# Kernel tuning notes

Hardware: AMD Instinct MI355X
Metric: run time of the kernel (lower is better)

## Reference

```python
import jax, jax.numpy as jnp
import numpy as np

DIM, HEADS, DHEAD, CTX_DIM, FF_MULT = 320, 8, 40, 768, 4
INNER_FF = FF_MULT * DIM  # 1280
EPS = 1e-5


def layer_norm(x, g, b):
    mu = jnp.mean(x, axis=-1, keepdims=True)
    var = jnp.mean((x - mu) ** 2, axis=-1, keepdims=True)
    return (x - mu) * jax.lax.rsqrt(var + EPS) * g + b


def attention(x, ctx, wq, wk, wv, wo, bo):
    # x: [b, i, DIM], ctx: [b, j, c]
    b, i, _ = x.shape
    j = ctx.shape[1]
    q = (x @ wq).reshape(b, i, HEADS, DHEAD)
    k = (ctx @ wk).reshape(b, j, HEADS, DHEAD)
    v = (ctx @ wv).reshape(b, j, HEADS, DHEAD)
    scale = DHEAD ** -0.5
    sim = jnp.einsum('bihd,bjhd->bhij', q, k) * scale  # full NxN, non-flash
    attn = jax.nn.softmax(sim, axis=-1)
    out = jnp.einsum('bhij,bjhd->bihd', attn, v).reshape(b, i, HEADS * DHEAD)
    return out @ wo + bo


def setup_inputs() -> dict:
    key = jax.random.key(0)
    ks = jax.random.split(key, 24)
    nrm = lambda k, shp, fan: jax.random.normal(k, shp, jnp.float32) * (fan ** -0.5)
    d = {
        'x': jax.random.normal(ks[0], (1, 4096, DIM), jnp.float32),
        'context': jax.random.normal(ks[1], (1, 77, CTX_DIM), jnp.float32),
        'n1_g': jnp.ones((DIM,), jnp.float32), 'n1_b': jnp.zeros((DIM,), jnp.float32),
        'a1_wq': nrm(ks[2], (DIM, DIM), DIM), 'a1_wk': nrm(ks[3], (DIM, DIM), DIM),
        'a1_wv': nrm(ks[4], (DIM, DIM), DIM), 'a1_wo': nrm(ks[5], (DIM, DIM), DIM),
        'a1_bo': jnp.zeros((DIM,), jnp.float32),
        'n2_g': jnp.ones((DIM,), jnp.float32), 'n2_b': jnp.zeros((DIM,), jnp.float32),
        'a2_wq': nrm(ks[6], (DIM, DIM), DIM), 'a2_wk': nrm(ks[7], (CTX_DIM, DIM), CTX_DIM),
        'a2_wv': nrm(ks[8], (CTX_DIM, DIM), CTX_DIM), 'a2_wo': nrm(ks[9], (DIM, DIM), DIM),
        'a2_bo': jnp.zeros((DIM,), jnp.float32),
        'n3_g': jnp.ones((DIM,), jnp.float32), 'n3_b': jnp.zeros((DIM,), jnp.float32),
        'ff_w1': nrm(ks[10], (DIM, 2 * INNER_FF), DIM),
        'ff_b1': jnp.zeros((2 * INNER_FF,), jnp.float32),
        'ff_w2': nrm(ks[11], (INNER_FF, DIM), INNER_FF),
        'ff_b2': jnp.zeros((DIM,), jnp.float32),
    }
    return d


def reference(x, context, n1_g, n1_b, a1_wq, a1_wk, a1_wv, a1_wo, a1_bo,
              n2_g, n2_b, a2_wq, a2_wk, a2_wv, a2_wo, a2_bo,
              n3_g, n3_b, ff_w1, ff_b1, ff_w2, ff_b2):
    # self-attention
    x = attention(layer_norm(x, n1_g, n1_b), layer_norm(x, n1_g, n1_b),
                  a1_wq, a1_wk, a1_wv, a1_wo, a1_bo) + x
    # cross-attention with text context
    x = attention(layer_norm(x, n2_g, n2_b), context,
                  a2_wq, a2_wk, a2_wv, a2_wo, a2_bo) + x
    # GEGLU feed-forward
    h = layer_norm(x, n3_g, n3_b) @ ff_w1 + ff_b1
    val, gate = jnp.split(h, 2, axis=-1)
    x = (val * jax.nn.gelu(gate, approximate=False)) @ ff_w2 + ff_b2 + x
    return x
```

## Files before the change

kernel.cpp:

```cpp
#include <hip/hip_runtime.h>
#include <hip/hip_bf16.h>
#include <math.h>

typedef __bf16 bf16;
typedef __attribute__((ext_vector_type(8))) __bf16 bf16x8;
typedef __attribute__((ext_vector_type(4))) __bf16 bf16x4;
typedef __attribute__((ext_vector_type(4))) float f32x4;
typedef __attribute__((ext_vector_type(2))) float f32x2;
typedef __attribute__((ext_vector_type(4))) short shortx4;

#define NTOK 4096
#define DIM  320
#define HEADS 8
#define DHEAD 40
#define NCTX 77
#define CTXD 768
#define IFF  1280

#define QSCALE (0.15811388300841897f * 1.4426950408889634f)

__device__ __forceinline__ bf16x8 bzero8() {
    bf16x8 v;
#pragma unroll
    for (int e = 0; e < 8; ++e) v[e] = (bf16)0.0f;
    return v;
}

__device__ __forceinline__ void gld_lds16(const void* g, void* l) {
    __builtin_amdgcn_global_load_lds(
        (const __attribute__((address_space(1))) void*)g,
        (__attribute__((address_space(3))) void*)l, 16, 0, 0);
}

#define PRE_TILES 2280
#define CONV_BLOCKS 231

struct PreJob { const float* src; bf16* dst; int K, N, ntx, tile0, perm; };
struct PreTab { PreJob j[10]; };

__global__ __launch_bounds__(256)
void preprocess_all(PreTab P, const float* __restrict__ ctx, bf16* __restrict__ ctxb) {
    const int b = blockIdx.x;
    const int tx = threadIdx.x, ty = threadIdx.y;
    if (b >= PRE_TILES) {
        int i = (b - PRE_TILES) * 256 + ty * 32 + tx;
        if (i < NCTX * CTXD) ctxb[i] = (bf16)ctx[i];
        return;
    }
    int ji = 0;
#pragma unroll
    for (int k = 1; k < 10; ++k)
        if (b >= P.j[k].tile0) ji = k;
    const PreJob jb = P.j[ji];
    const int local = b - jb.tile0;
    const int n0 = (local % jb.ntx) * 32;
    const int k0 = (local / jb.ntx) * 32;

    __shared__ float tile[32][33];
#pragma unroll
    for (int i = 0; i < 4; ++i)
        tile[ty + i * 8][tx] = jb.src[(size_t)(k0 + ty + i * 8) * jb.N + n0 + tx];
    __syncthreads();
#pragma unroll
    for (int i = 0; i < 4; ++i) {
        int n = n0 + ty + i * 8;
        int nd = jb.perm ? ((n < 1280) ? 2 * n : 2 * (n - 1280) + 1) : n;
        jb.dst[(size_t)nd * jb.K + k0 + tx] = (bf16)tile[tx][ty + i * 8];
    }
}

__device__ __forceinline__ void ln_body(const float* __restrict__ X, const float* __restrict__ g,
                                        const float* __restrict__ b, bf16* __restrict__ Y, int row) {
    int lane = threadIdx.x & 63;
    const float* xr = X + (size_t)row * DIM;
    float v[5];
    float sum = 0.f;
#pragma unroll
    for (int c = 0; c < 5; ++c) { v[c] = xr[c * 64 + lane]; sum += v[c]; }
#pragma unroll
    for (int off = 1; off < 64; off <<= 1) sum += __shfl_xor(sum, off);
    float mu = sum * (1.f / 320.f);
    float vs = 0.f;
#pragma unroll
    for (int c = 0; c < 5; ++c) { float d = v[c] - mu; vs += d * d; }
#pragma unroll
    for (int off = 1; off < 64; off <<= 1) vs += __shfl_xor(vs, off);
    float rs = rsqrtf(vs * (1.f / 320.f) + 1e-5f);
    bf16* yr = Y + (size_t)row * DIM;
#pragma unroll
    for (int c = 0; c < 5; ++c)
        yr[c * 64 + lane] = (bf16)((v[c] - mu) * rs * g[c * 64 + lane] + b[c * 64 + lane]);
}

__global__ __launch_bounds__(256)
void layernorm_kernel(const float* __restrict__ X, const float* __restrict__ g,
                      const float* __restrict__ b, bf16* __restrict__ Y) {
    ln_body(X, g, b, Y, blockIdx.x * 4 + (threadIdx.x >> 6));
}

template <int EPI, int BM, int BN, int SWZ>
__global__ __launch_bounds__(256)
void gemm_db(const bf16* __restrict__ A, const bf16* __restrict__ Bt,
             int M, int N, int K,
             bf16* __restrict__ Y0, bf16* __restrict__ Y1, bf16* __restrict__ Y2,
             float* Yf, const float* __restrict__ bias, const float* res, int trs) {
    constexpr int ABYTES = BM * 128;
    constexpr int BBYTES = BN * 128;
    constexpr int FB = ABYTES + BBYTES;
    constexpr int WM = BM / 2;
    constexpr int WN = BN / 2;
    constexpr int MI = WM / 16;
    constexpr int NI = WN / 16;
    constexpr int ACH = BM / 32;
    constexpr int BCH = BN / 32;
    __shared__ char smem[2 * FB];
    const int t = threadIdx.x, lane = t & 63, w = t >> 6;
    const int wr = w >> 1, wc = w & 1;

    int bx = blockIdx.x, by = blockIdx.y;
    if (SWZ) {
        int gx = gridDim.x;
        int nwg = gx * gridDim.y;
        int bid = by * gx + bx;
        int s = (bid & 7) * (nwg >> 3) + (bid >> 3);
        bx = s % gx; by = s / gx;
    }
    const int m0 = bx * BM;
    const int n0 = by * BN;

    const bf16* asrc[ACH];
    const bf16* bsrc[BCH];
#pragma unroll
    for (int i = 0; i < ACH; ++i) {
        int ch = i * 256 + t;
        int row = ch >> 3, seg = (ch & 7) ^ (row & 7);
        asrc[i] = A + (size_t)(m0 + row) * K + seg * 8;
    }
#pragma unroll
    for (int i = 0; i < BCH; ++i) {
        int ch = i * 256 + t;
        int row = ch >> 3, seg = (ch & 7) ^ (row & 7);
        bsrc[i] = Bt + (size_t)(n0 + row) * K + seg * 8;
    }

    f32x4 acc[MI][NI];
#pragma unroll
    for (int mi = 0; mi < MI; ++mi)
#pragma unroll
        for (int ni = 0; ni < NI; ++ni)
#pragma unroll
            for (int r = 0; r < 4; ++r) acc[mi][ni][r] = 0.f;

    auto STAGE = [&](char* base, int k0) {
#pragma unroll
        for (int i = 0; i < ACH; ++i)
            gld_lds16(asrc[i] + k0, base + (i * 256 + w * 64) * 16);
#pragma unroll
        for (int i = 0; i < BCH; ++i)
            gld_lds16(bsrc[i] + k0, base + ABYTES + (i * 256 + w * 64) * 16);
    };

    char* cur = smem;
    char* nxt = smem + FB;
    STAGE(cur, 0);
    __syncthreads();

    for (int k0 = 0; k0 < K; k0 += 64) {
        if (k0 + 64 < K) STAGE(nxt, k0 + 64);
        bf16x8 a[MI][2], b[NI][2];
#pragma unroll
        for (int mi = 0; mi < MI; ++mi)
#pragma unroll
            for (int kh = 0; kh < 2; ++kh) {
                int row = wr * WM + mi * 16 + (lane & 15);
                a[mi][kh] = *(const bf16x8*)(cur + row * 128 +
                             ((kh * 64 + (lane >> 4) * 16) ^ ((row & 7) << 4)));
            }
#pragma unroll
        for (int ni = 0; ni < NI; ++ni)
#pragma unroll
            for (int kh = 0; kh < 2; ++kh) {
                int row = wc * WN + ni * 16 + (lane & 15);
                b[ni][kh] = *(const bf16x8*)(cur + ABYTES + row * 128 +
                             ((kh * 64 + (lane >> 4) * 16) ^ ((row & 7) << 4)));
            }
#pragma unroll
        for (int mi = 0; mi < MI; ++mi)
#pragma unroll
            for (int ni = 0; ni < NI; ++ni) {
                acc[mi][ni] = __builtin_amdgcn_mfma_f32_16x16x32_bf16(a[mi][0], b[ni][0], acc[mi][ni], 0, 0, 0);
                acc[mi][ni] = __builtin_amdgcn_mfma_f32_16x16x32_bf16(a[mi][1], b[ni][1], acc[mi][ni], 0, 0, 0);
            }
        __syncthreads();
        char* tmp = cur; cur = nxt; nxt = tmp;
    }

#pragma unroll
    for (int mi = 0; mi < MI; ++mi)
#pragma unroll
        for (int ni = 0; ni < NI; ++ni) {
            const int col = n0 + wc * WN + ni * 16 + (lane & 15);
            const int rowb = m0 + wr * WM + mi * 16 + (lane >> 4) * 4;
            if (EPI == 5) {
                if (col < 320) {
#pragma unroll
                    for (int r = 0; r < 4; ++r)
                        Y0[(size_t)(rowb + r) * 320 + col] = (bf16)(acc[mi][ni][r] * QSCALE);
                } else if (col < 640) {
#pragma unroll
                    for (int r = 0; r < 4; ++r)
                        Y1[(size_t)(rowb + r) * 320 + (col - 320)] = (bf16)acc[mi][ni][r];
                } else {
                    bf16x4 tv;
#pragma unroll
                    for (int r = 0; r < 4; ++r) tv[r] = (bf16)acc[mi][ni][r];
                    *(bf16x4*)(Y2 + (size_t)(col - 640) * trs + rowb) = tv;
                }
            } else if (EPI == 7) {
                int bidx = (col & 1) ? (1280 + (col >> 1)) : (col >> 1);
                float bc = bias[bidx];
#pragma unroll
                for (int r = 0; r < 4; ++r) {
                    float v = acc[mi][ni][r] + bc;
                    float other = __shfl_xor(v, 1);
                    if (!(col & 1)) {
                        float gl = 0.5f * other * (1.f + erff(other * 0.70710678118654752f));
                        Y0[(size_t)(rowb + r) * 1280 + (col >> 1)] = (bf16)(v * gl);
                    }
                }
            } else {
#pragma unroll
                for (int r = 0; r < 4; ++r) {
                    int row = rowb + r;
                    if (row < M) {
                        float v = acc[mi][ni][r];
                        if (EPI == 4) Y0[(size_t)row * N + col] = (bf16)(v * QSCALE);
                        else Yf[(size_t)row * N + col] = v + bias[col] + res[(size_t)row * N + col];
                    }
                }
            }
        }
}

__global__ __launch_bounds__(256)
void ln2_plus_cross(const float* __restrict__ X, const float* __restrict__ g,
                    const float* __restrict__ bb, bf16* __restrict__ Y,
                    const bf16* __restrict__ A, const bf16* __restrict__ Bt,
                    bf16* __restrict__ Y0, bf16* __restrict__ Y2, int trs) {
    __shared__ char smem[24 * 1024];
    if (blockIdx.x < 1024) {
        ln_body(X, g, bb, Y, blockIdx.x * 4 + (threadIdx.x >> 6));
        return;
    }
    const int M = NCTX, K = CTXD;
    const int t = threadIdx.x;
    const int lane = t & 63;
    const int w = t >> 6;
    const int wr = w >> 1, wc = w & 1;
    const int n0 = (blockIdx.x - 1024) * 64;

    f32x4 acc[4][2];
#pragma unroll
    for (int mi = 0; mi < 4; ++mi)
#pragma unroll
        for (int ni = 0; ni < 2; ++ni)
#pragma unroll
            for (int r = 0; r < 4; ++r) acc[mi][ni][r] = 0.f;

    for (int k0 = 0; k0 < K; k0 += 64) {
#pragma unroll
        for (int i = 0; i < 4; ++i) {
            int c = t + i * 256;
            int row = c >> 3, seg = c & 7;
            bf16x8 v = bzero8();
            if (row < M) v = *(const bf16x8*)(A + (size_t)row * K + k0 + seg * 8);
            *(bf16x8*)(smem + row * 128 + ((seg * 16) ^ ((row & 7) << 4))) = v;
        }
#pragma unroll
        for (int i = 0; i < 2; ++i) {
            int c = t + i * 256;
            int row = c >> 3, seg = c & 7;
            bf16x8 v = *(const bf16x8*)(Bt + (size_t)(n0 + row) * K + k0 + seg * 8);
            *(bf16x8*)(smem + 16 * 1024 + row * 128 + ((seg * 16) ^ ((row & 7) << 4))) = v;
        }
        __syncthreads();

        bf16x8 a[4][2], bfr[2][2];
#pragma unroll
        for (int mi = 0; mi < 4; ++mi)
#pragma unroll
            for (int kh = 0; kh < 2; ++kh) {
                int row = wr * 64 + mi * 16 + (lane & 15);
                a[mi][kh] = *(const bf16x8*)(smem + row * 128 +
                             ((kh * 64 + (lane >> 4) * 16) ^ ((row & 7) << 4)));
            }
#pragma unroll
        for (int ni = 0; ni < 2; ++ni)
#pragma unroll
            for (int kh = 0; kh < 2; ++kh) {
                int row = wc * 32 + ni * 16 + (lane & 15);
                bfr[ni][kh] = *(const bf16x8*)(smem + 16 * 1024 + row * 128 +
                               ((kh * 64 + (lane >> 4) * 16) ^ ((row & 7) << 4)));
            }
#pragma unroll
        for (int mi = 0; mi < 4; ++mi)
#pragma unroll
            for (int ni = 0; ni < 2; ++ni) {
                acc[mi][ni] = __builtin_amdgcn_mfma_f32_16x16x32_bf16(a[mi][0], bfr[ni][0], acc[mi][ni], 0, 0, 0);
                acc[mi][ni] = __builtin_amdgcn_mfma_f32_16x16x32_bf16(a[mi][1], bfr[ni][1], acc[mi][ni], 0, 0, 0);
            }
        __syncthreads();
    }

#pragma unroll
    for (int mi = 0; mi < 4; ++mi)
#pragma unroll
        for (int ni = 0; ni < 2; ++ni) {
            const int col = n0 + wc * 32 + ni * 16 + (lane & 15);
            const int rowb = wr * 64 + mi * 16 + (lane >> 4) * 4;
            if (col < 320) {
#pragma unroll
                for (int r = 0; r < 4; ++r)
                    if (rowb + r < M) Y0[(size_t)(rowb + r) * 320 + col] = (bf16)acc[mi][ni][r];
            } else {
                bf16x4 tv;
#pragma unroll
                for (int r = 0; r < 4; ++r) tv[r] = (bf16)acc[mi][ni][r];
                *(bf16x4*)(Y2 + (size_t)(col - 320) * trs + rowb) = tv;
            }
        }
}

#define KVT 64
#define KBYTES 5120
#define VBYTES 6144
#define FBUF (KBYTES + VBYTES)

template <int DIRECT>
__global__ __launch_bounds__(256, 4)
void flash_attn5(const bf16* __restrict__ Qg, const bf16* __restrict__ Kg,
                 const bf16* __restrict__ VTg, bf16* __restrict__ O,
                 float* __restrict__ Opart, float* __restrict__ MLpart,
                 int nkv, int vstride, int tiles_per_split) {
    __shared__ char smem[2 * FBUF];
    const int t = threadIdx.x, lane = t & 63, w = t >> 6;
    const int g = lane >> 4, q = lane & 15;
    const int h = blockIdx.y, split = blockIdx.z;
    const int qb = blockIdx.x * 64 + w * 16;

    const int ntiles = (nkv + KVT - 1) / KVT;
    const int tt0 = split * tiles_per_split;
    int tt1 = tt0 + tiles_per_split;
    if (tt1 > ntiles) tt1 = ntiles;

    if (t < 128) {
        bf16x8 v = bzero8();
        if (((t & 63) >> 3) == 0) {
#pragma unroll
            for (int e = 0; e < 8; ++e) v[e] = (bf16)1.0f;
        }
        *(bf16x8*)(smem + (t >> 6) * FBUF + KBYTES + 5120 + (t & 63) * 16) = v;
    }

    const int nslot = (w == 3) ? 1 : 3;
    const bf16* srcp[3];
    int dstoff[3], sstep[3];
#pragma unroll
    for (int s = 0; s < 3; ++s) {
        int id = w * 3 + s;
        if (id < 5) {
            int c16 = id * 64 + lane;
            int row = c16 / 5, seg = c16 - row * 5;
            srcp[s] = Kg + (size_t)(tt0 * KVT + row) * DIM + h * DHEAD + seg * 8;
            sstep[s] = KVT * DIM;
            dstoff[s] = id * 1024;
        } else {
            int vv = id - 5;
            int c16 = vv * 64 + lane;
            int row = c16 >> 3, seg = (c16 & 7) ^ (row & 7);
            srcp[s] = VTg + (size_t)(h * DHEAD + row) * vstride + tt0 * KVT + seg * 8;
            sstep[s] = KVT;
            dstoff[s] = KBYTES + vv * 1024;
        }
    }

#define STAGE(BUFOFF)                                                     \
    do {                                                                  \
        _Pragma("unroll")                                                 \
        for (int s = 0; s < 3; ++s) {                                     \
            if (s < nslot) {                                              \
                gld_lds16(srcp[s], smem + (BUFOFF) + dstoff[s]);          \
                srcp[s] += sstep[s];                                      \
            }                                                             \
        }                                                                 \
    } while (0)

    bf16x8 qf0 = *(const bf16x8*)(Qg + (size_t)(qb + q) * DIM + h * DHEAD + g * 8);
    bf16x8 qf1 = bzero8();
    if (g == 0) qf1 = *(const bf16x8*)(Qg + (size_t)(qb + q) * DIM + h * DHEAD + 32);

    f32x4 accO[3];
#pragma unroll
    for (int dt = 0; dt < 3; ++dt)
#pragma unroll
        for (int r = 0; r < 4; ++r) accO[dt][r] = 0.f;
    float m_run = -1e30f;

#define TILE_BODY(KSC, J0)                                                        \
    do {                                                                          \
        const char* Ks_ = (KSC);                                                  \
        const char* Vs_ = Ks_ + KBYTES;                                           \
        f32x4 s4[4];                                                              \
        __builtin_amdgcn_s_setprio(1);                                            \
        _Pragma("unroll")                                                         \
        for (int jt = 0; jt < 4; ++jt) {                                          \
            const char* krow = Ks_ + (jt * 16 + q) * 80;                          \
            bf16x8 kb0 = *(const bf16x8*)(krow + g * 16);                         \
            bf16x8 kb1 = bzero8();                                                \
            if (g == 0) kb1 = *(const bf16x8*)(krow + 64);                        \
            f32x4 z;                                                              \
            _Pragma("unroll") for (int r = 0; r < 4; ++r) z[r] = 0.f;             \
            z = __builtin_amdgcn_mfma_f32_16x16x32_bf16(kb0, qf0, z, 0, 0, 0);    \
            z = __builtin_amdgcn_mfma_f32_16x16x32_bf16(kb1, qf1, z, 0, 0, 0);    \
            s4[jt] = z;                                                           \
        }                                                                         \
        __builtin_amdgcn_s_setprio(0);                                            \
        if ((J0) + KVT > nkv) {                                                   \
            _Pragma("unroll") for (int jt = 0; jt < 4; ++jt)                      \
            _Pragma("unroll") for (int r = 0; r < 4; ++r)                         \
                if ((J0) + jt * 16 + g * 4 + r >= nkv) s4[jt][r] = -1e30f;        \
        }                                                                         \
        f32x4 mvv = s4[0];                                                        \
        _Pragma("unroll") for (int jt = 1; jt < 4; ++jt)                          \
        _Pragma("unroll") for (int r = 0; r < 4; ++r)                             \
            mvv[r] = fmaxf(mvv[r], s4[jt][r]);                                    \
        float mt = fmaxf(fmaxf(mvv[0], mvv[1]), fmaxf(mvv[2], mvv[3]));           \
        mt = fmaxf(mt, __shfl_xor(mt, 16));                                       \
        mt = fmaxf(mt, __shfl_xor(mt, 32));                                       \
        if (!__all(mt <= m_run + 8.f)) {                                          \
            float mnew = fmaxf(m_run, mt);                                        \
            float f = exp2f(m_run - mnew);                                        \
            m_run = mnew;                                                         \
            _Pragma("unroll") for (int dt = 0; dt < 3; ++dt)                      \
            _Pragma("unroll") for (int r = 0; r < 4; ++r) accO[dt][r] *= f;       \
        }                                                                         \
        union PU { bf16x4 hv; shortx4 sv; } pk[4];                                \
        _Pragma("unroll") for (int jt = 0; jt < 4; ++jt) {                        \
            bf16x4 hv;                                                            \
            _Pragma("unroll") for (int r = 0; r < 4; ++r)                         \
                hv[r] = (bf16)exp2f(s4[jt][r] - m_run);                           \
            pk[jt].hv = hv;                                                       \
        }                                                                         \
        __builtin_amdgcn_s_setprio(1);                                            \
        _Pragma("unroll") for (int dt = 0; dt < 3; ++dt) {                        \
            const char* vrow = Vs_ + (dt * 16 + q) * 128;                         \
            _Pragma("unroll") for (int jt = 0; jt < 4; ++jt) {                    \
                shortx4 vb = *(const shortx4*)(vrow +                             \
                               ((jt * 32 + g * 8) ^ ((q & 7) << 4)));             \
                accO[dt] = __builtin_amdgcn_mfma_f32_16x16x16bf16_1k(             \
                               vb, pk[jt].sv, accO[dt], 0, 0, 0);                 \
            }                                                                     \
        }                                                                         \
        __builtin_amdgcn_s_setprio(0);                                            \
        __syncthreads();                                                          \
    } while (0)

    STAGE(0);
    __syncthreads();

    int tt = tt0;
    while (tt < tt1) {
        if (tt + 1 < tt1) STAGE(FBUF);
        TILE_BODY(smem, tt * KVT);
        ++tt;
        if (tt >= tt1) break;
        if (tt + 1 < tt1) STAGE(0);
        TILE_BODY(smem + FBUF, tt * KVT);
        ++tt;
    }
#undef TILE_BODY
#undef STAGE

    float l = __shfl(accO[2][0], 32 + q);

    if (DIRECT) {
        float inv = 1.f / l;
#pragma unroll
        for (int dt = 0; dt < 3; ++dt) {
            if (dt < 2 || g < 2) {
                bf16x4 o;
#pragma unroll
                for (int r = 0; r < 4; ++r) o[r] = (bf16)(accO[dt][r] * inv);
                *(bf16x4*)(O + (size_t)(qb + q) * DIM + h * DHEAD + dt * 16 + g * 4) = o;
            }
        }
    } else {
        size_t rowi = (size_t)(split * HEADS + h) * NTOK + qb + q;
#pragma unroll
        for (int dt = 0; dt < 3; ++dt) {
            if (dt < 2 || g < 2)
                *(f32x4*)(Opart + rowi * 40 + dt * 16 + g * 4) = accO[dt];
        }
        if (g == 2) {
            f32x2 ml;
            ml[0] = m_run; ml[1] = accO[2][0];
            *(f32x2*)(MLpart + rowi * 2) = ml;
        }
    }
}

__global__ __launch_bounds__(256)
void flash_combine(const float* __restrict__ Opart, const float* __restrict__ MLpart,
                   bf16* __restrict__ O) {
    int idx = blockIdx.x * 256 + threadIdx.x;
    int qi = idx / 40, c = idx - qi * 40;
    int h = c / 5, c8 = c - h * 5;
    float mv[4], lv[4];
    float M = -1e30f;
#pragma unroll
    for (int s = 0; s < 4; ++s) {
        f32x2 ml = *(const f32x2*)(MLpart + ((size_t)(s * HEADS + h) * NTOK + qi) * 2);
        mv[s] = ml[0]; lv[s] = ml[1];
        M = fmaxf(M, ml[0]);
    }
    float wgt[4], denom = 0.f;
#pragma unroll
    for (int s = 0; s < 4; ++s) { wgt[s] = exp2f(mv[s] - M); denom += wgt[s] * lv[s]; }
    float inv = 1.f / denom;
    float o[8];
#pragma unroll
    for (int e = 0; e < 8; ++e) o[e] = 0.f;
#pragma unroll
    for (int s = 0; s < 4; ++s) {
        const float* op = Opart + ((size_t)(s * HEADS + h) * NTOK + qi) * 40 + c8 * 8;
#pragma unroll
        for (int e = 0; e < 8; ++e) o[e] += wgt[s] * op[e];
    }
    bf16x8 ov;
#pragma unroll
    for (int e = 0; e < 8; ++e) ov[e] = (bf16)(o[e] * inv);
    *(bf16x8*)(O + (size_t)qi * DIM + h * DHEAD + c8 * 8) = ov;
}

extern "C" void kernel_launch(void* const* d_in, const int* in_sizes, int n_in,
                              void* d_out, int out_size, void* d_ws, size_t ws_size,
                              hipStream_t stream) {
    const float* x     = (const float*)d_in[0];
    const float* ctx   = (const float*)d_in[1];
    const float* n1_g  = (const float*)d_in[2];
    const float* n1_b  = (const float*)d_in[3];
    const float* a1_wq = (const float*)d_in[4];
    const float* a1_wk = (const float*)d_in[5];
    const float* a1_wv = (const float*)d_in[6];
    const float* a1_wo = (const float*)d_in[7];
    const float* a1_bo = (const float*)d_in[8];
    const float* n2_g  = (const float*)d_in[9];
    const float* n2_b  = (const float*)d_in[10];
    const float* a2_wq = (const float*)d_in[11];
    const float* a2_wk = (const float*)d_in[12];
    const float* a2_wv = (const float*)d_in[13];
    const float* a2_wo = (const float*)d_in[14];
    const float* a2_bo = (const float*)d_in[15];
    const float* n3_g  = (const float*)d_in[16];
    const float* n3_b  = (const float*)d_in[17];
    const float* ff_w1 = (const float*)d_in[18];
    const float* ff_b1 = (const float*)d_in[19];
    const float* ff_w2 = (const float*)d_in[20];
    const float* ff_b2 = (const float*)d_in[21];

    char* ws = (char*)d_ws;
    size_t off = 0;
    auto alloc = [&](size_t bytes) -> char* {
        char* p = ws + off;
        off += (bytes + 255) & ~(size_t)255;
        return p;
    };
    bf16* lnbuf  = (bf16*)alloc((size_t)NTOK * DIM * 2);
    bf16* qbuf   = (bf16*)alloc((size_t)NTOK * DIM * 2);
    bf16* kbuf   = (bf16*)alloc((size_t)NTOK * DIM * 2);
    bf16* vtbuf  = (bf16*)alloc((size_t)DIM * NTOK * 2);
    bf16* abuf   = (bf16*)alloc((size_t)NTOK * DIM * 2);
    bf16* hbuf   = (bf16*)alloc((size_t)NTOK * 2 * IFF * 2);
    bf16* gbuf   = (bf16*)alloc((size_t)NTOK * IFF * 2);
    bf16* ctxb   = (bf16*)alloc((size_t)NCTX * CTXD * 2);
    bf16* k2buf  = (bf16*)alloc((size_t)128 * DIM * 2);
    bf16* vt2buf = (bf16*)alloc((size_t)DIM * 128 * 2);
    bf16* wqkvT  = (bf16*)alloc((size_t)960 * DIM * 2);
    bf16* woT    = (bf16*)alloc((size_t)DIM * DIM * 2);
    bf16* q2T    = (bf16*)alloc((size_t)DIM * DIM * 2);
    bf16* wkv2T  = (bf16*)alloc((size_t)640 * CTXD * 2);
    bf16* o2T    = (bf16*)alloc((size_t)DIM * DIM * 2);
    bf16* w1T    = (bf16*)alloc((size_t)2 * IFF * DIM * 2);
    bf16* w2T    = (bf16*)alloc((size_t)IFF * DIM * 2);
    float* out   = (float*)d_out;

    float* Opart  = (float*)hbuf;
    float* MLpart = (float*)gbuf;

    {
        PreTab P;
        auto set = [&](int i, const float* s, bf16* d, int K, int N, int tile0, int perm) {
            P.j[i].src = s; P.j[i].dst = d; P.j[i].K = K; P.j[i].N = N;
            P.j[i].ntx = N / 32; P.j[i].tile0 = tile0; P.j[i].perm = perm;
        };
        set(0, a1_wq, wqkvT,                        320, 320,    0, 0);
        set(1, a1_wk, wqkvT + (size_t)320 * 320,    320, 320,  100, 0);
        set(2, a1_wv, wqkvT + (size_t)640 * 320,    320, 320,  200, 0);
        set(3, a1_wo, woT,                          320, 320,  300, 0);
        set(4, a2_wq, q2T,                          320, 320,  400, 0);
        set(5, a2_wo, o2T,                          320, 320,  500, 0);
        set(6, a2_wk, wkv2T,                        768, 320,  600, 0);
        set(7, a2_wv, wkv2T + (size_t)320 * 768,    768, 320,  840, 0);
        set(8, ff_w1, w1T,                          320, 2560, 1080, 1);
        set(9, ff_w2, w2T,                          1280, 320, 1880, 0);
        preprocess_all<<<PRE_TILES + CONV_BLOCKS, dim3(32, 8), 0, stream>>>(P, ctx, ctxb);
    }

    layernorm_kernel<<<1024, 256, 0, stream>>>(x, n1_g, n1_b, lnbuf);
    gemm_db<5, 128, 64, 1><<<dim3(32, 15), 256, 0, stream>>>(lnbuf, wqkvT, NTOK, 960, DIM,
                                                             qbuf, kbuf, vtbuf, nullptr, nullptr, nullptr, NTOK);
    flash_attn5<0><<<dim3(64, 8, 4), 256, 0, stream>>>(qbuf, kbuf, vtbuf, nullptr,
                                                       Opart, MLpart, NTOK, NTOK, 16);
    flash_combine<<<640, 256, 0, stream>>>(Opart, MLpart, abuf);
    gemm_db<2, 64, 64, 1><<<dim3(64, 5), 256, 0, stream>>>(abuf, woT, NTOK, DIM, DIM,
                                                           nullptr, nullptr, nullptr, out, a1_bo, x, 0);

    ln2_plus_cross<<<1034, 256, 0, stream>>>(out, n2_g, n2_b, lnbuf,
                                             ctxb, wkv2T, k2buf, vt2buf, 128);
    gemm_db<4, 64, 64, 1><<<dim3(64, 5), 256, 0, stream>>>(lnbuf, q2T, NTOK, DIM, DIM,
                                                           qbuf, nullptr, nullptr, nullptr, nullptr, nullptr, 0);
    flash_attn5<1><<<dim3(64, 8, 1), 256, 0, stream>>>(qbuf, k2buf, vt2buf, abuf,
                                                       nullptr, nullptr, NCTX, 128, 2);
    gemm_db<2, 64, 64, 1><<<dim3(64, 5), 256, 0, stream>>>(abuf, o2T, NTOK, DIM, DIM,
                                                           nullptr, nullptr, nullptr, out, a2_bo, out, 0);

    layernorm_kernel<<<1024, 256, 0, stream>>>(out, n3_g, n3_b, lnbuf);
    gemm_db<7, 128, 64, 1><<<dim3(32, 40), 256, 0, stream>>>(lnbuf, w1T, NTOK, 2 * IFF, DIM,
                                                             gbuf, nullptr, nullptr, nullptr, ff_b1, nullptr, 0);
    gemm_db<2, 64, 64, 1><<<dim3(64, 5), 256, 0, stream>>>(gbuf, w2T, NTOK, DIM, IFF,
                                                           nullptr, nullptr, nullptr, out, ff_b2, out, 0);
}
```

Baseline: 187.2 us.

## Double flash-attention KV tile to 128 and fold LN1 into preprocess kernel

Raises the flash-attention KV tile from 64 to 128 keys, resizing the K/V shared buffers, the staging map (5 loads per wave, so all waves now share the load work) and the V transpose swizzle. Tiles per split are halved to keep the same coverage. Separately, the first layernorm is merged into the weight-preprocess launch as extra blocks, removing one kernel launch. The larger tile means fewer barriers and loop iterations but more registers and shared memory per block, which may lower occupancy under the 4-blocks-per-CU bound.

```diff
diff --git a/kernel.cpp b/kernel.cpp
--- a/kernel.cpp
+++ b/kernel.cpp
@@ -32,21 +32,58 @@
         (__attribute__((address_space(3))) void*)l, 16, 0, 0);
 }
 
+__device__ __forceinline__ void ln_body(const float* __restrict__ X, const float* __restrict__ g,
+                                        const float* __restrict__ b, bf16* __restrict__ Y, int row) {
+    int lane = threadIdx.x & 63;
+    const float* xr = X + (size_t)row * DIM;
+    float v[5];
+    float sum = 0.f;
+#pragma unroll
+    for (int c = 0; c < 5; ++c) { v[c] = xr[c * 64 + lane]; sum += v[c]; }
+#pragma unroll
+    for (int off = 1; off < 64; off <<= 1) sum += __shfl_xor(sum, off);
+    float mu = sum * (1.f / 320.f);
+    float vs = 0.f;
+#pragma unroll
+    for (int c = 0; c < 5; ++c) { float d = v[c] - mu; vs += d * d; }
+#pragma unroll
+    for (int off = 1; off < 64; off <<= 1) vs += __shfl_xor(vs, off);
+    float rs = rsqrtf(vs * (1.f / 320.f) + 1e-5f);
+    bf16* yr = Y + (size_t)row * DIM;
+#pragma unroll
+    for (int c = 0; c < 5; ++c)
+        yr[c * 64 + lane] = (bf16)((v[c] - mu) * rs * g[c * 64 + lane] + b[c * 64 + lane]);
+}
+
+__global__ __launch_bounds__(256)
+void layernorm_kernel(const float* __restrict__ X, const float* __restrict__ g,
+                      const float* __restrict__ b, bf16* __restrict__ Y) {
+    ln_body(X, g, b, Y, blockIdx.x * 4 + (threadIdx.x >> 6));
+}
+
 #define PRE_TILES 2280
 #define CONV_BLOCKS 231
+#define LN1_BLOCKS 1024
 
 struct PreJob { const float* src; bf16* dst; int K, N, ntx, tile0, perm; };
 struct PreTab { PreJob j[10]; };
 
 __global__ __launch_bounds__(256)
-void preprocess_all(PreTab P, const float* __restrict__ ctx, bf16* __restrict__ ctxb) {
+void preprocess_all(PreTab P, const float* __restrict__ ctx, bf16* __restrict__ ctxb,
+                    const float* __restrict__ x, const float* __restrict__ n1_g,
+                    const float* __restrict__ n1_b, bf16* __restrict__ lnbuf) {
     const int b = blockIdx.x;
-    const int tx = threadIdx.x, ty = threadIdx.y;
+    const int t = threadIdx.x;
+    if (b >= PRE_TILES + CONV_BLOCKS) {
+        ln_body(x, n1_g, n1_b, lnbuf, (b - PRE_TILES - CONV_BLOCKS) * 4 + (t >> 6));
+        return;
+    }
     if (b >= PRE_TILES) {
-        int i = (b - PRE_TILES) * 256 + ty * 32 + tx;
+        int i = (b - PRE_TILES) * 256 + t;
         if (i < NCTX * CTXD) ctxb[i] = (bf16)ctx[i];
         return;
     }
+    const int tx = t & 31, ty = t >> 5;
     int ji = 0;
 #pragma unroll
     for (int k = 1; k < 10; ++k)
@@ -67,35 +104,6 @@
         int nd = jb.perm ? ((n < 1280) ? 2 * n : 2 * (n - 1280) + 1) : n;
         jb.dst[(size_t)nd * jb.K + k0 + tx] = (bf16)tile[tx][ty + i * 8];
     }
-}
-
-__device__ __forceinline__ void ln_body(const float* __restrict__ X, const float* __restrict__ g,
-                                        const float* __restrict__ b, bf16* __restrict__ Y, int row) {
-    int lane = threadIdx.x & 63;
-    const float* xr = X + (size_t)row * DIM;
-    float v[5];
-    float sum = 0.f;
-#pragma unroll
-    for (int c = 0; c < 5; ++c) { v[c] = xr[c * 64 + lane]; sum += v[c]; }
-#pragma unroll
-    for (int off = 1; off < 64; off <<= 1) sum += __shfl_xor(sum, off);
-    float mu = sum * (1.f / 320.f);
-    float vs = 0.f;
-#pragma unroll
-    for (int c = 0; c < 5; ++c) { float d = v[c] - mu; vs += d * d; }
-#pragma unroll
-    for (int off = 1; off < 64; off <<= 1) vs += __shfl_xor(vs, off);
-    float rs = rsqrtf(vs * (1.f / 320.f) + 1e-5f);
-    bf16* yr = Y + (size_t)row * DIM;
-#pragma unroll
-    for (int c = 0; c < 5; ++c)
-        yr[c * 64 + lane] = (bf16)((v[c] - mu) * rs * g[c * 64 + lane] + b[c * 64 + lane]);
-}
-
-__global__ __launch_bounds__(256)
-void layernorm_kernel(const float* __restrict__ X, const float* __restrict__ g,
-                      const float* __restrict__ b, bf16* __restrict__ Y) {
-    ln_body(X, g, b, Y, blockIdx.x * 4 + (threadIdx.x >> 6));
 }
 
 template <int EPI, int BM, int BN, int SWZ>
@@ -331,14 +339,14 @@
         }
 }
 
-#define KVT 64
-#define KBYTES 5120
-#define VBYTES 6144
+#define KVT 128
+#define KBYTES 10240
+#define VBYTES 12288
 #define FBUF (KBYTES + VBYTES)
 
 template <int DIRECT>
 __global__ __launch_bounds__(256, 4)
-void flash_attn5(const bf16* __restrict__ Qg, const bf16* __restrict__ Kg,
+void flash_attn7(const bf16* __restrict__ Qg, const bf16* __restrict__ Kg,
                  const bf16* __restrict__ VTg, bf16* __restrict__ O,
                  float* __restrict__ Opart, float* __restrict__ MLpart,
                  int nkv, int vstride, int tiles_per_split) {
@@ -353,31 +361,32 @@
     int tt1 = tt0 + tiles_per_split;
     if (tt1 > ntiles) tt1 = ntiles;
 
-    if (t < 128) {
+    {
+        int buf = t >> 7, idx = t & 127;
+        int row = 40 + (idx >> 4), seg = idx & 15;
         bf16x8 v = bzero8();
-        if (((t & 63) >> 3) == 0) {
+        if ((idx >> 4) == 0) {
 #pragma unroll
             for (int e = 0; e < 8; ++e) v[e] = (bf16)1.0f;
         }
-        *(bf16x8*)(smem + (t >> 6) * FBUF + KBYTES + 5120 + (t & 63) * 16) = v;
-    }
-
-    const int nslot = (w == 3) ? 1 : 3;
-    const bf16* srcp[3];
-    int dstoff[3], sstep[3];
-#pragma unroll
-    for (int s = 0; s < 3; ++s) {
-        int id = w * 3 + s;
-        if (id < 5) {
+        *(bf16x8*)(smem + buf * FBUF + KBYTES + row * 256 + seg * 16) = v;
+    }
+
+    const bf16* srcp[5];
+    int dstoff[5], sstep[5];
+#pragma unroll
+    for (int s = 0; s < 5; ++s) {
+        int id = w * 5 + s;
+        if (id < 10) {
             int c16 = id * 64 + lane;
             int row = c16 / 5, seg = c16 - row * 5;
             srcp[s] = Kg + (size_t)(tt0 * KVT + row) * DIM + h * DHEAD + seg * 8;
             sstep[s] = KVT * DIM;
             dstoff[s] = id * 1024;
         } else {
-            int vv = id - 5;
+            int vv = id - 10;
             int c16 = vv * 64 + lane;
-            int row = c16 >> 3, seg = (c16 & 7) ^ (row & 7);
+            int row = c16 >> 4, seg = (c16 & 15) ^ (row & 7);
             srcp[s] = VTg + (size_t)(h * DHEAD + row) * vstride + tt0 * KVT + seg * 8;
             sstep[s] = KVT;
             dstoff[s] = KBYTES + vv * 1024;
@@ -387,11 +396,9 @@
 #define STAGE(BUFOFF)                                                     \
     do {                                                                  \
         _Pragma("unroll")                                                 \
-        for (int s = 0; s < 3; ++s) {                                     \
-            if (s < nslot) {                                              \
-                gld_lds16(srcp[s], smem + (BUFOFF) + dstoff[s]);          \
-                srcp[s] += sstep[s];                                      \
-            }                                                             \
+        for (int s = 0; s < 5; ++s) {                                     \
+            gld_lds16(srcp[s], smem + (BUFOFF) + dstoff[s]);              \
+            srcp[s] += sstep[s];                                          \
         }                                                                 \
     } while (0)
 
@@ -410,10 +417,10 @@
     do {                                                                          \
         const char* Ks_ = (KSC);                                                  \
         const char* Vs_ = Ks_ + KBYTES;                                           \
-        f32x4 s4[4];                                                              \
+        f32x4 s4[8];                                                              \
         __builtin_amdgcn_s_setprio(1);                                            \
         _Pragma("unroll")                                                         \
-        for (int jt = 0; jt < 4; ++jt) {                                          \
+        for (int jt = 0; jt < 8; ++jt) {                                          \
             const char* krow = Ks_ + (jt * 16 + q) * 80;                          \
             bf16x8 kb0 = *(const bf16x8*)(krow + g * 16);                         \
             bf16x8 kb1 = bzero8();                                                \
@@ -426,12 +433,12 @@
         }                                                                         \
         __builtin_amdgcn_s_setprio(0);                                            \
         if ((J0) + KVT > nkv) {                                                   \
-            _Pragma("unroll") for (int jt = 0; jt < 4; ++jt)                      \
+            _Pragma("unroll") for (int jt = 0; jt < 8; ++jt)                      \
             _Pragma("unroll") for (int r = 0; r < 4; ++r)                         \
                 if ((J0) + jt * 16 + g * 4 + r >= nkv) s4[jt][r] = -1e30f;        \
         }                                                                         \
         f32x4 mvv = s4[0];                                                        \
-        _Pragma("unroll") for (int jt = 1; jt < 4; ++jt)                          \
+        _Pragma("unroll") for (int jt = 1; jt < 8; ++jt)                          \
         _Pragma("unroll") for (int r = 0; r < 4; ++r)                             \
             mvv[r] = fmaxf(mvv[r], s4[jt][r]);                                    \
         float mt = fmaxf(fmaxf(mvv[0], mvv[1]), fmaxf(mvv[2], mvv[3]));           \
@@ -444,8 +451,8 @@
             _Pragma("unroll") for (int dt = 0; dt < 3; ++dt)                      \
             _Pragma("unroll") for (int r = 0; r < 4; ++r) accO[dt][r] *= f;       \
         }                                                                         \
-        union PU { bf16x4 hv; shortx4 sv; } pk[4];                                \
-        _Pragma("unroll") for (int jt = 0; jt < 4; ++jt) {                        \
+        union PU { bf16x4 hv; shortx4 sv; } pk[8];                                \
+        _Pragma("unroll") for (int jt = 0; jt < 8; ++jt) {                        \
             bf16x4 hv;                                                            \
             _Pragma("unroll") for (int r = 0; r < 4; ++r)                         \
                 hv[r] = (bf16)exp2f(s4[jt][r] - m_run);                           \
@@ -453,8 +460,8 @@
         }                                                                         \
         __builtin_amdgcn_s_setprio(1);                                            \
         _Pragma("unroll") for (int dt = 0; dt < 3; ++dt) {                        \
-            const char* vrow = Vs_ + (dt * 16 + q) * 128;                         \
-            _Pragma("unroll") for (int jt = 0; jt < 4; ++jt) {                    \
+            const char* vrow = Vs_ + (dt * 16 + q) * 256;                         \
+            _Pragma("unroll") for (int jt = 0; jt < 8; ++jt) {                    \
                 shortx4 vb = *(const shortx4*)(vrow +                             \
                                ((jt * 32 + g * 8) ^ ((q & 7) << 4)));             \
                 accO[dt] = __builtin_amdgcn_mfma_f32_16x16x16bf16_1k(             \
@@ -613,14 +620,14 @@
         set(7, a2_wv, wkv2T + (size_t)320 * 768,    768, 320,  840, 0);
         set(8, ff_w1, w1T,                          320, 2560, 1080, 1);
         set(9, ff_w2, w2T,                          1280, 320, 1880, 0);
-        preprocess_all<<<PRE_TILES + CONV_BLOCKS, dim3(32, 8), 0, stream>>>(P, ctx, ctxb);
-    }
-
-    layernorm_kernel<<<1024, 256, 0, stream>>>(x, n1_g, n1_b, lnbuf);
+        preprocess_all<<<PRE_TILES + CONV_BLOCKS + LN1_BLOCKS, 256, 0, stream>>>(
+            P, ctx, ctxb, x, n1_g, n1_b, lnbuf);
+    }
+
     gemm_db<5, 128, 64, 1><<<dim3(32, 15), 256, 0, stream>>>(lnbuf, wqkvT, NTOK, 960, DIM,
                                                              qbuf, kbuf, vtbuf, nullptr, nullptr, nullptr, NTOK);
-    flash_attn5<0><<<dim3(64, 8, 4), 256, 0, stream>>>(qbuf, kbuf, vtbuf, nullptr,
-                                                       Opart, MLpart, NTOK, NTOK, 16);
+    flash_attn7<0><<<dim3(64, 8, 4), 256, 0, stream>>>(qbuf, kbuf, vtbuf, nullptr,
+                                                       Opart, MLpart, NTOK, NTOK, 8);
     flash_combine<<<640, 256, 0, stream>>>(Opart, MLpart, abuf);
     gemm_db<2, 64, 64, 1><<<dim3(64, 5), 256, 0, stream>>>(abuf, woT, NTOK, DIM, DIM,
                                                            nullptr, nullptr, nullptr, out, a1_bo, x, 0);
@@ -629,8 +636,8 @@
                                              ctxb, wkv2T, k2buf, vt2buf, 128);
     gemm_db<4, 64, 64, 1><<<dim3(64, 5), 256, 0, stream>>>(lnbuf, q2T, NTOK, DIM, DIM,
                                                            qbuf, nullptr, nullptr, nullptr, nullptr, nullptr, 0);
-    flash_attn5<1><<<dim3(64, 8, 1), 256, 0, stream>>>(qbuf, k2buf, vt2buf, abuf,
-                                                       nullptr, nullptr, NCTX, 128, 2);
+    flash_attn7<1><<<dim3(64, 8, 1), 256, 0, stream>>>(qbuf, k2buf, vt2buf, abuf,
+                                                       nullptr, nullptr, NCTX, 128, 1);
     gemm_db<2, 64, 64, 1><<<dim3(64, 5), 256, 0, stream>>>(abuf, o2T, NTOK, DIM, DIM,
                                                            nullptr, nullptr, nullptr, out, a2_bo, out, 0);
 
```

After: 190.4 us. About the same (+1.7%).
